# Kernel tuning notes

Measured on AMD Instinct MI355X. Metric: run time of the kernel, lower is better.

Reference implementation:

```python
import jax, jax.numpy as jnp
import numpy as np

SCALE = 1.0  # module scale=1; dropout_p=0 so dropout is identity; selector is Identity


def setup_inputs() -> dict:
    key = jax.random.key(0)
    k0, k1, k2, k3, k4 = jax.random.split(key, 5)
    B, S, DIN, DOUT, P, R = 4, 2048, 4096, 4096, 5, 8
    x = jax.random.normal(k0, (B, S, DIN), dtype=jnp.float32)
    W = jax.random.normal(k1, (DOUT, DIN), dtype=jnp.float32) * 0.02   # nn.Linear weight [out, in]
    lora_down = jax.random.normal(k2, (P, DIN, R), dtype=jnp.float32) * 0.02
    lora_up = jax.random.normal(k3, (P, R, DOUT), dtype=jnp.float32) * 0.02
    lora_route = jax.random.normal(k4, (P, DIN, P), dtype=jnp.float32) * 0.02
    return {"x": x, "W": W, "lora_down": lora_down, "lora_up": lora_up,
            "lora_route": lora_route, "task_id": 4}


def reference(x, W, lora_down, lora_up, lora_route, task_id):
    tid = task_id  # Python int (static), tid > 1 branch
    # Routing: logits over the first (tid-1) experts using route table of task tid
    logits = jnp.einsum('bsi,ij->bsj', x, lora_route[tid - 1, :, :tid - 1])  # [B,S,tid-1]
    omegas = jax.nn.softmax(logits, axis=-1)
    # Previous experts: (lora_down[j] @ lora_up[j]).detach() -> stop_gradient.
    # Keep low-rank structure: z = x @ down  [B,S,J,R], then weight and project up.
    down_prev = jax.lax.stop_gradient(lora_down[:tid - 1])  # [J, DIN, R]
    up_prev = jax.lax.stop_gradient(lora_up[:tid - 1])      # [J, R, DOUT]
    z = jnp.einsum('bsi,jir->bsjr', x, down_prev)           # [B,S,J,R] small (R=8)
    delta_prev = jnp.einsum('bsjr,jro->bso', z * omegas[..., None], up_prev)
    # Current expert (j == tid-1): live params, no gating weight
    cur = (x @ lora_down[tid - 1]) @ lora_up[tid - 1]       # [B,S,DOUT]
    delta = SCALE * (delta_prev + cur)
    return x @ W.T + delta
```

## Files before the change

kernel.cpp:

```cpp
#include <hip/hip_runtime.h>
#include <hip/hip_bf16.h>

typedef unsigned short u16;
typedef __attribute__((ext_vector_type(8))) __bf16 bf16x8;
typedef __attribute__((ext_vector_type(4))) float f32x4;

#define DIN 4096
#define DOUT 4096
#define MROWS 8192

__device__ __forceinline__ u16 f2bf(float f) {
  unsigned int u = __float_as_uint(f);
  u += 0x7fffu + ((u >> 16) & 1u);
  return (u16)(u >> 16);
}

__device__ __forceinline__ void gl2lds16(const void* g, void* l) {
  __builtin_amdgcn_global_load_lds(
      (const __attribute__((address_space(1))) unsigned int*)g,
      (__attribute__((address_space(3))) unsigned int*)l, 16, 0, 0);
}

__global__ __launch_bounds__(256) void convx(const float* __restrict__ x,
                                             u16* __restrict__ Xb) {
  size_t i = ((size_t)blockIdx.x * 256 + threadIdx.x) * 4;
  float4 v = *(const float4*)(x + i);
  ushort4 o;
  o.x = f2bf(v.x); o.y = f2bf(v.y); o.z = f2bf(v.z); o.w = f2bf(v.w);
  *(ushort4*)(Xb + i) = o;
}

__global__ __launch_bounds__(256) void convw(const float* __restrict__ W,
                                             u16* __restrict__ Wb) {
  size_t i = ((size_t)blockIdx.x * 256 + threadIdx.x) * 4;
  float4 v = *(const float4*)(W + i);
  ushort4 o;
  o.x = f2bf(v.x); o.y = f2bf(v.y); o.z = f2bf(v.z); o.w = f2bf(v.w);
  *(ushort4*)(Wb + i) = o;
}

__global__ __launch_bounds__(256) void convu(const float* __restrict__ up,
                                             u16* __restrict__ Ub) {
  int n = blockIdx.x * 256 + threadIdx.x;
  union { u16 us[32]; uint4 q[4]; } o;
  #pragma unroll
  for (int c = 0; c < 32; ++c) o.us[c] = f2bf(up[(size_t)c * DOUT + n]);
  uint4* dst = (uint4*)(Ub + (size_t)n * 32);
  #pragma unroll
  for (int q = 0; q < 4; ++q) dst[q] = o.q[q];
}

__global__ __launch_bounds__(256) void wtprep(const float* __restrict__ route,
                                              const float* __restrict__ down,
                                              u16* __restrict__ Wt) {
  const int c = blockIdx.y;
  const int k0 = blockIdx.x * 1024 + threadIdx.x * 4;
  const float* route3 = route + 3 * DIN * 5;
  float v[4];
  #pragma unroll
  for (int j = 0; j < 4; ++j) {
    int k = k0 + j;
    float f;
    if (c < 3)       f = route3[(size_t)k * 5 + c];
    else if (c < 35) f = down[(size_t)((c - 3) >> 3) * DIN * 8 + (size_t)k * 8 + ((c - 3) & 7)];
    else             f = 0.f;
    v[j] = f;
  }
  ushort4 o;
  o.x = f2bf(v[0]); o.y = f2bf(v[1]); o.z = f2bf(v[2]); o.w = f2bf(v[3]);
  *(ushort4*)(Wt + (size_t)c * DIN + k0) = o;
}

__global__ __launch_bounds__(256) void coeffgemm(
    const u16* __restrict__ Xb, const u16* __restrict__ Wt,
    float* __restrict__ Pw) {
  __shared__ __align__(16) u16 As[128 * 64];
  __shared__ __align__(16) u16 Bs[48 * 64];
  const int tid = threadIdx.x;
  const int m0 = blockIdx.x * 128;
  const int kb = blockIdx.y * 512;
  const int lane = tid & 63;
  const int w = tid >> 6;
  const int wr = w * 32;
  const int fm = lane & 15;
  const int xr = fm & 7;
  const int qd = lane >> 4;

  f32x4 acc[2][3];
  #pragma unroll
  for (int i = 0; i < 2; ++i)
    #pragma unroll
    for (int j = 0; j < 3; ++j) acc[i][j] = (f32x4){0.f, 0.f, 0.f, 0.f};

  const int srow = tid >> 3;
  const int scol = ((tid & 7) ^ (srow & 7)) * 8;
  const u16* gA = Xb + (size_t)(m0 + srow) * DIN + kb + scol;
  u16* lA = As + tid * 8;

  for (int kc = 0; kc < 512; kc += 64) {
    gl2lds16(Wt + (size_t)srow * DIN + kb + kc + scol, Bs + tid * 8);
    if (tid < 128) {
      int u = 256 + tid;
      int usw = ((u & 7) ^ ((u >> 3) & 7)) * 8;
      gl2lds16(Wt + (size_t)(u >> 3) * DIN + kb + kc + usw, Bs + u * 8);
    }
    #pragma unroll
    for (int it = 0; it < 4; ++it)
      gl2lds16(gA + kc + (size_t)(it * 32) * DIN, lA + it * 2048);
    __syncthreads();
    #pragma unroll
    for (int kk = 0; kk < 64; kk += 32) {
      const int q = (kk >> 3) + qd;
      bf16x8 af[2], bfr[3];
      #pragma unroll
      for (int i = 0; i < 2; ++i)
        af[i] = *(const bf16x8*)(As + (wr + i * 16 + fm) * 64 + ((q ^ xr) << 3));
      #pragma unroll
      for (int j = 0; j < 3; ++j)
        bfr[j] = *(const bf16x8*)(Bs + (j * 16 + fm) * 64 + ((q ^ xr) << 3));
      #pragma unroll
      for (int i = 0; i < 2; ++i)
        #pragma unroll
        for (int j = 0; j < 3; ++j)
          acc[i][j] = __builtin_amdgcn_mfma_f32_16x16x32_bf16(af[i], bfr[j], acc[i][j], 0, 0, 0);
    }
    __syncthreads();
  }
  const int em = (lane >> 4) * 4;
  const int en = lane & 15;
  const size_t pbase = (size_t)blockIdx.y * MROWS;
  #pragma unroll
  for (int i = 0; i < 2; ++i)
    #pragma unroll
    for (int j = 0; j < 3; ++j)
      #pragma unroll
      for (int r = 0; r < 4; ++r)
        Pw[(pbase + m0 + wr + i * 16 + em + r) * 48 + j * 16 + en] = acc[i][j][r];
}

__global__ __launch_bounds__(256) void reduce_coeff(const float* __restrict__ Pw,
                                                    u16* __restrict__ Cb) {
  const int m = blockIdx.x * 256 + threadIdx.x;
  float s[48];
  #pragma unroll
  for (int c = 0; c < 48; ++c) s[c] = 0.f;
  for (int sp = 0; sp < 8; ++sp) {
    const float4* p = (const float4*)(Pw + ((size_t)sp * MROWS + m) * 48);
    #pragma unroll
    for (int q = 0; q < 12; ++q) {
      float4 v = p[q];
      s[q * 4 + 0] += v.x; s[q * 4 + 1] += v.y;
      s[q * 4 + 2] += v.z; s[q * 4 + 3] += v.w;
    }
  }
  float mx = fmaxf(s[0], fmaxf(s[1], s[2]));
  float e0 = __expf(s[0] - mx), e1 = __expf(s[1] - mx), e2 = __expf(s[2] - mx);
  float inv = 1.f / (e0 + e1 + e2);
  float om0 = e0 * inv, om1 = e1 * inv, om2 = e2 * inv;
  union { u16 us[32]; uint4 q[4]; } o;
  #pragma unroll
  for (int c = 0; c < 32; ++c) {
    float wgt = (c < 8) ? om0 : (c < 16) ? om1 : (c < 24) ? om2 : 1.f;
    o.us[c] = f2bf(s[3 + c] * wgt);
  }
  uint4* dst = (uint4*)(Cb + (size_t)m * 32);
  #pragma unroll
  for (int q = 0; q < 4; ++q) dst[q] = o.q[q];
}


#define MF(a, b, c) __builtin_amdgcn_mfma_f32_16x16x32_bf16(a, b, c, 0, 0, 0)

#define MROW(A, I) \
  acc[I][0] = MF(A, bfr0, acc[I][0]); \
  acc[I][1] = MF(A, bfr1, acc[I][1]); \
  acc[I][2] = MF(A, bfr2, acc[I][2]); \
  acc[I][3] = MF(A, bfr3, acc[I][3]);

#define VM4 asm volatile("s_waitcnt vmcnt(4)" ::: "memory")
#define VM0 asm volatile("s_waitcnt vmcnt(0)" ::: "memory")

#define STA(REG, KOFF) { const u16* s_ = gA + (KOFF); \
  gl2lds16(s_, dA + (REG) * 8192); \
  gl2lds16(s_ + 128 * 4096, dA + (REG) * 8192 + 4096); }
#define STB(REG, KOFF) { const u16* s_ = gB + (KOFF); \
  gl2lds16(s_, dB + (REG) * 8192); \
  gl2lds16(s_ + 128 * 4096, dB + (REG) * 8192 + 4096); }
#define STC { const u16* s_ = Cb + (size_t)(m0 + gr1) * 32 + kc1; \
  gl2lds16(s_, dA); gl2lds16(s_ + 128 * 32, dA + 4096); }
#define STU { const u16* s_ = Ub + (size_t)(n0 + gr1) * 32 + kc1; \
  gl2lds16(s_, dB); gl2lds16(s_ + 128 * 32, dB + 4096); }

#define PH(REG, IH, LOADB, ISSUE, VMX) { \
  const u16* ap_ = sm + (REG) * 8192 + wmoff + (IH) * 2048 + off0; \
  bf16x8 af0 = *(const bf16x8*)(ap_); \
  bf16x8 af1 = *(const bf16x8*)(ap_ + 512); \
  bf16x8 af2 = *(const bf16x8*)(ap_ + 1024); \
  bf16x8 af3 = *(const bf16x8*)(ap_ + 1536); \
  if (LOADB) { \
    const u16* bp_ = sm + 32768 + (REG) * 8192 + wnoff + off0; \
    bfr0 = *(const bf16x8*)(bp_); \
    bfr1 = *(const bf16x8*)(bp_ + 512); \
    bfr2 = *(const bf16x8*)(bp_ + 1024); \
    bfr3 = *(const bf16x8*)(bp_ + 1536); \
  } \
  ISSUE; \
  asm volatile("" ::: "memory"); \
  __builtin_amdgcn_s_barrier(); \
  __builtin_amdgcn_s_setprio(1); \
  MROW(af0, (IH) * 4 + 0) \
  MROW(af1, (IH) * 4 + 1) \
  MROW(af2, (IH) * 4 + 2) \
  MROW(af3, (IH) * 4 + 3) \
  __builtin_amdgcn_s_setprio(0); \
  VMX; \
  asm volatile("" ::: "memory"); \
  __builtin_amdgcn_s_barrier(); \
}

#define TILE(B, I1, I2, I3, I4, VMX) { \
  bf16x8 bfr0, bfr1, bfr2, bfr3; \
  PH((B) * 2 + 0, 0, 1, I1, (void)0) \
  PH((B) * 2 + 0, 1, 0, I2, (void)0) \
  PH((B) * 2 + 1, 0, 1, I3, (void)0) \
  PH((B) * 2 + 1, 1, 0, I4, VMX) \
}

__global__ __launch_bounds__(512, 2) void gemm_fused8(
    const u16* __restrict__ Xb, const u16* __restrict__ Wb,
    const u16* __restrict__ Cb, const u16* __restrict__ Ub,
    float* __restrict__ out) {
  __shared__ __align__(16) u16 sm[65536];
  const int tid = threadIdx.x;
  const int bid = blockIdx.x;
  const int wg = (bid & 7) * 64 + (bid >> 3);
  const int mt = wg >> 4;
  const int nt = wg & 15;
  const int m0 = mt * 256;
  const int n0 = nt * 256;
  const int lane = tid & 63;
  const int w = tid >> 6;
  const int wm = w >> 2;
  const int wn = w & 3;
  const int fm = lane & 15;
  const int qd = lane >> 4;
  const int off0 = (fm >> 1) * 64 + (((((fm & 1) << 2) | qd)) ^ (fm >> 1)) * 8;
  const int wmoff = wm * 4096;
  const int wnoff = wn * 2048;

  const int c1 = (tid & 7) ^ ((tid >> 3) & 7);
  const int gr1 = 2 * (tid >> 3) + (c1 >> 2);
  const int kc1 = (c1 & 3) * 8;
  const u16* gA = Xb + (size_t)(m0 + gr1) * 4096 + kc1;
  const u16* gB = Wb + (size_t)(n0 + gr1) * 4096 + kc1;
  u16* dA = sm + tid * 8;
  u16* dB = sm + 32768 + tid * 8;

  f32x4 acc[8][4];
  #pragma unroll
  for (int i = 0; i < 8; ++i)
    #pragma unroll
    for (int j = 0; j < 4; ++j) acc[i][j] = (f32x4){0.f, 0.f, 0.f, 0.f};

  STA(0, 0)  STB(0, 0)
  STA(1, 32) STB(1, 32)
  STA(2, 64) STB(2, 64)
  VM4;
  asm volatile("" ::: "memory");
  __builtin_amdgcn_s_barrier();

  for (int T = 0; T < 62; T += 2) {
    TILE(0, STA(3, T * 64 + 96),  STB(3, T * 64 + 96),
            STA(0, T * 64 + 128), STB(0, T * 64 + 128), VM4)
    TILE(1, STA(1, T * 64 + 160), STB(1, T * 64 + 160),
            STA(2, T * 64 + 192), STB(2, T * 64 + 192), VM4)
  }
  TILE(0, STA(3, 4064), STB(3, 4064), (void)0, (void)0, VM0)
  TILE(1, STC, STU, (void)0, (void)0, VM0)

  {
    const u16* ap = sm + wmoff + off0;
    const u16* bp = sm + 32768 + wnoff + off0;
    bf16x8 bfr0 = *(const bf16x8*)(bp);
    bf16x8 bfr1 = *(const bf16x8*)(bp + 512);
    bf16x8 bfr2 = *(const bf16x8*)(bp + 1024);
    bf16x8 bfr3 = *(const bf16x8*)(bp + 1536);
    #pragma unroll
    for (int i = 0; i < 8; ++i) {
      bf16x8 a = *(const bf16x8*)(ap + i * 512);
      acc[i][0] = MF(a, bfr0, acc[i][0]);
      acc[i][1] = MF(a, bfr1, acc[i][1]);
      acc[i][2] = MF(a, bfr2, acc[i][2]);
      acc[i][3] = MF(a, bfr3, acc[i][3]);
    }
  }

  const int em = qd * 4;
  const int en = fm;
  const size_t obase = (size_t)(m0 + wm * 128) * DOUT + n0 + wn * 64 + en;
  #pragma unroll
  for (int i = 0; i < 8; ++i)
    #pragma unroll
    for (int j = 0; j < 4; ++j)
      #pragma unroll
      for (int r = 0; r < 4; ++r)
        out[obase + (size_t)(i * 16 + em + r) * DOUT + j * 16] = acc[i][j][r];
}

extern "C" void kernel_launch(void* const* d_in, const int* in_sizes, int n_in,
                              void* d_out, int out_size, void* d_ws, size_t ws_size,
                              hipStream_t stream) {
  const float* x     = (const float*)d_in[0];
  const float* W     = (const float*)d_in[1];
  const float* down  = (const float*)d_in[2];
  const float* up    = (const float*)d_in[3];
  const float* route = (const float*)d_in[4];
  float* out = (float*)d_out;

  char* ws = (char*)d_ws;
  u16*   Xb = (u16*)ws;
  u16*   Wb = (u16*)(ws + 67108864);
  u16*   Cb = (u16*)(ws + 100663296);
  u16*   Ub = (u16*)(ws + 101187584);
  u16*   Wt = (u16*)(ws + 101449728);
  float* Pw = (float*)(ws + 101842944);

  convx<<<32768, 256, 0, stream>>>(x, Xb);
  convw<<<16384, 256, 0, stream>>>(W, Wb);
  convu<<<16, 256, 0, stream>>>(up, Ub);
  wtprep<<<dim3(4, 48), 256, 0, stream>>>(route, down, Wt);
  coeffgemm<<<dim3(64, 8), 256, 0, stream>>>(Xb, Wt, Pw);
  reduce_coeff<<<32, 256, 0, stream>>>(Pw, Cb);
  gemm_fused8<<<512, 512, 0, stream>>>(Xb, Wb, Cb, Ub, out);
}
```

Before: 521.7 us.

## Merge GEMM half-phases into one barrier phase per K-slice and parallelize coefficient reduce

The main GEMM now runs one phase per K-slice. Each phase loads all eight A fragments and four B fragments, then issues 32 MFMAs between barriers, instead of two half-phases of 16. This halves the barrier count and the points where a global-to-LDS load is issued, but it doubles the A fragment registers live at once, which may pressure occupancy at 2 waves/SIMD. The coefficient reduce kernel now splits each row across four threads with shuffles for the softmax logits. That gives 4x more blocks and smaller per-thread register arrays, at the cost of scalar bf16 stores.

Result: no change. 512.7 us (-1.7%).

```diff
diff --git a/kernel.cpp b/kernel.cpp
--- a/kernel.cpp
+++ b/kernel.cpp
@@ -20,6 +20,7 @@
       (const __attribute__((address_space(1))) unsigned int*)g,
       (__attribute__((address_space(3))) unsigned int*)l, 16, 0, 0);
 }
+
 
 __global__ __launch_bounds__(256) void convx(const float* __restrict__ x,
                                              u16* __restrict__ Xb) {
@@ -140,32 +141,40 @@
 
 __global__ __launch_bounds__(256) void reduce_coeff(const float* __restrict__ Pw,
                                                     u16* __restrict__ Cb) {
-  const int m = blockIdx.x * 256 + threadIdx.x;
-  float s[48];
-  #pragma unroll
-  for (int c = 0; c < 48; ++c) s[c] = 0.f;
+  const int tid = threadIdx.x;
+  const int rl = tid >> 2;
+  const int cg = tid & 3;
+  const int m = blockIdx.x * 64 + rl;
+  const int lane = tid & 63;
+
+  float s[12];
+  #pragma unroll
+  for (int q = 0; q < 12; ++q) s[q] = 0.f;
   for (int sp = 0; sp < 8; ++sp) {
-    const float4* p = (const float4*)(Pw + ((size_t)sp * MROWS + m) * 48);
-    #pragma unroll
-    for (int q = 0; q < 12; ++q) {
+    const float4* p = (const float4*)(Pw + ((size_t)sp * MROWS + m) * 48 + cg * 12);
+    #pragma unroll
+    for (int q = 0; q < 3; ++q) {
       float4 v = p[q];
       s[q * 4 + 0] += v.x; s[q * 4 + 1] += v.y;
       s[q * 4 + 2] += v.z; s[q * 4 + 3] += v.w;
     }
   }
-  float mx = fmaxf(s[0], fmaxf(s[1], s[2]));
-  float e0 = __expf(s[0] - mx), e1 = __expf(s[1] - mx), e2 = __expf(s[2] - mx);
-  float inv = 1.f / (e0 + e1 + e2);
-  float om0 = e0 * inv, om1 = e1 * inv, om2 = e2 * inv;
-  union { u16 us[32]; uint4 q[4]; } o;
-  #pragma unroll
-  for (int c = 0; c < 32; ++c) {
-    float wgt = (c < 8) ? om0 : (c < 16) ? om1 : (c < 24) ? om2 : 1.f;
-    o.us[c] = f2bf(s[3 + c] * wgt);
-  }
-  uint4* dst = (uint4*)(Cb + (size_t)m * 32);
-  #pragma unroll
-  for (int q = 0; q < 4; ++q) dst[q] = o.q[q];
+  const int src = lane & ~3;
+  const float L0 = __shfl(s[0], src);
+  const float L1 = __shfl(s[1], src);
+  const float L2 = __shfl(s[2], src);
+  const float mx = fmaxf(L0, fmaxf(L1, L2));
+  const float e0 = __expf(L0 - mx), e1 = __expf(L1 - mx), e2 = __expf(L2 - mx);
+  const float inv = 1.f / (e0 + e1 + e2);
+  const float om0 = e0 * inv, om1 = e1 * inv, om2 = e2 * inv;
+  #pragma unroll
+  for (int j = 0; j < 12; ++j) {
+    const int G = cg * 12 + j;
+    if (G >= 3 && G < 35) {
+      const float wgt = (G < 11) ? om0 : (G < 19) ? om1 : (G < 27) ? om2 : 1.f;
+      Cb[(size_t)m * 32 + (G - 3)] = f2bf(s[j] * wgt);
+    }
+  }
 }
 
 
@@ -186,44 +195,43 @@
 #define STB(REG, KOFF) { const u16* s_ = gB + (KOFF); \
   gl2lds16(s_, dB + (REG) * 8192); \
   gl2lds16(s_ + 128 * 4096, dB + (REG) * 8192 + 4096); }
+#define STAB(REG, KOFF) { STA(REG, KOFF) STB(REG, KOFF) }
 #define STC { const u16* s_ = Cb + (size_t)(m0 + gr1) * 32 + kc1; \
   gl2lds16(s_, dA); gl2lds16(s_ + 128 * 32, dA + 4096); }
 #define STU { const u16* s_ = Ub + (size_t)(n0 + gr1) * 32 + kc1; \
   gl2lds16(s_, dB); gl2lds16(s_ + 128 * 32, dB + 4096); }
-
-#define PH(REG, IH, LOADB, ISSUE, VMX) { \
-  const u16* ap_ = sm + (REG) * 8192 + wmoff + (IH) * 2048 + off0; \
+#define STCU { STC STU }
+
+#define PH2(REG, ISSUE, VMX) { \
+  const u16* ap_ = sm + (REG) * 8192 + wmoff + off0; \
   bf16x8 af0 = *(const bf16x8*)(ap_); \
   bf16x8 af1 = *(const bf16x8*)(ap_ + 512); \
   bf16x8 af2 = *(const bf16x8*)(ap_ + 1024); \
   bf16x8 af3 = *(const bf16x8*)(ap_ + 1536); \
-  if (LOADB) { \
-    const u16* bp_ = sm + 32768 + (REG) * 8192 + wnoff + off0; \
-    bfr0 = *(const bf16x8*)(bp_); \
-    bfr1 = *(const bf16x8*)(bp_ + 512); \
-    bfr2 = *(const bf16x8*)(bp_ + 1024); \
-    bfr3 = *(const bf16x8*)(bp_ + 1536); \
-  } \
+  bf16x8 af4 = *(const bf16x8*)(ap_ + 2048); \
+  bf16x8 af5 = *(const bf16x8*)(ap_ + 2560); \
+  bf16x8 af6 = *(const bf16x8*)(ap_ + 3072); \
+  bf16x8 af7 = *(const bf16x8*)(ap_ + 3584); \
+  const u16* bp_ = sm + 32768 + (REG) * 8192 + wnoff + off0; \
+  bf16x8 bfr0 = *(const bf16x8*)(bp_); \
+  bf16x8 bfr1 = *(const bf16x8*)(bp_ + 512); \
+  bf16x8 bfr2 = *(const bf16x8*)(bp_ + 1024); \
+  bf16x8 bfr3 = *(const bf16x8*)(bp_ + 1536); \
   ISSUE; \
   asm volatile("" ::: "memory"); \
   __builtin_amdgcn_s_barrier(); \
   __builtin_amdgcn_s_setprio(1); \
-  MROW(af0, (IH) * 4 + 0) \
-  MROW(af1, (IH) * 4 + 1) \
-  MROW(af2, (IH) * 4 + 2) \
-  MROW(af3, (IH) * 4 + 3) \
+  MROW(af0, 0) MROW(af1, 1) MROW(af2, 2) MROW(af3, 3) \
+  MROW(af4, 4) MROW(af5, 5) MROW(af6, 6) MROW(af7, 7) \
   __builtin_amdgcn_s_setprio(0); \
   VMX; \
   asm volatile("" ::: "memory"); \
   __builtin_amdgcn_s_barrier(); \
 }
 
-#define TILE(B, I1, I2, I3, I4, VMX) { \
-  bf16x8 bfr0, bfr1, bfr2, bfr3; \
-  PH((B) * 2 + 0, 0, 1, I1, (void)0) \
-  PH((B) * 2 + 0, 1, 0, I2, (void)0) \
-  PH((B) * 2 + 1, 0, 1, I3, (void)0) \
-  PH((B) * 2 + 1, 1, 0, I4, VMX) \
+#define TILE2(B, I1, I2, VMX) { \
+  PH2((B) * 2 + 0, I1, (void)0) \
+  PH2((B) * 2 + 1, I2, VMX) \
 }
 
 __global__ __launch_bounds__(512, 2) void gemm_fused8(
@@ -270,13 +278,11 @@
   __builtin_amdgcn_s_barrier();
 
   for (int T = 0; T < 62; T += 2) {
-    TILE(0, STA(3, T * 64 + 96),  STB(3, T * 64 + 96),
-            STA(0, T * 64 + 128), STB(0, T * 64 + 128), VM4)
-    TILE(1, STA(1, T * 64 + 160), STB(1, T * 64 + 160),
-            STA(2, T * 64 + 192), STB(2, T * 64 + 192), VM4)
-  }
-  TILE(0, STA(3, 4064), STB(3, 4064), (void)0, (void)0, VM0)
-  TILE(1, STC, STU, (void)0, (void)0, VM0)
+    TILE2(0, STAB(3, T * 64 + 96),  STAB(0, T * 64 + 128), VM4)
+    TILE2(1, STAB(1, T * 64 + 160), STAB(2, T * 64 + 192), VM4)
+  }
+  TILE2(0, STAB(3, 4064), (void)0, VM0)
+  TILE2(1, STCU, (void)0, VM0)
 
   {
     const u16* ap = sm + wmoff + off0;
@@ -330,6 +336,6 @@
   convu<<<16, 256, 0, stream>>>(up, Ub);
   wtprep<<<dim3(4, 48), 256, 0, stream>>>(route, down, Wt);
   coeffgemm<<<dim3(64, 8), 256, 0, stream>>>(Xb, Wt, Pw);
-  reduce_coeff<<<32, 256, 0, stream>>>(Pw, Cb);
+  reduce_coeff<<<128, 256, 0, stream>>>(Pw, Cb);
   gemm_fused8<<<512, 512, 0, stream>>>(Xb, Wb, Cb, Ub, out);
 }
```
